# Kernel tuning notes

Measured on AMD Instinct MI355X. Metric: run time of the kernel, lower is better.

The kernel has to match this reference:

```python
import jax, jax.numpy as jnp
import numpy as np

N_AGENTS = 32
UNIT_DIM = 32
STATE_DIM = 1200
N_HEAD = 8
EMBED = 64
KEY_HID = 2 * EMBED
HYPER = 256
V_HID = 4 * EMBED
ATTEND_REG_COEF = 0.001
BS, T = 128, 32


def setup_inputs() -> dict:
    key = jax.random.key(0)
    ks = jax.random.split(key, 12)
    def lin(k, shape, fan_in):
        return jax.random.normal(k, shape, jnp.float32) / np.sqrt(fan_in)
    return dict(
        agent_qs=jax.random.normal(ks[0], (BS, T, N_AGENTS), jnp.float32),
        states=jax.random.normal(ks[1], (BS, T, STATE_DIM), jnp.float32),
        actions=jax.random.randint(ks[2], (BS, T, N_AGENTS), 0, 20),
        sel_W1=lin(ks[3], (N_HEAD, HYPER, STATE_DIM), STATE_DIM),
        sel_b1=jnp.zeros((N_HEAD, HYPER), jnp.float32),
        sel_W2=lin(ks[4], (N_HEAD, EMBED, HYPER), HYPER),
        key_W1=lin(ks[5], (N_HEAD, KEY_HID, UNIT_DIM + 1), UNIT_DIM + 1),
        key_b1=jnp.zeros((N_HEAD, KEY_HID), jnp.float32),
        key_W2=lin(ks[6], (N_HEAD, EMBED, KEY_HID), KEY_HID),
        wh_W1=lin(ks[7], (HYPER, STATE_DIM), STATE_DIM),
        wh_b1=jnp.zeros((HYPER,), jnp.float32),
        wh_W2=lin(ks[8], (N_HEAD, HYPER), HYPER),
        wh_b2=jnp.zeros((N_HEAD,), jnp.float32),
        v_W1=lin(ks[9], (V_HID, STATE_DIM), STATE_DIM),
        v_b1=jnp.zeros((V_HID,), jnp.float32),
        v_W2=lin(ks[10], (1, V_HID), V_HID),
        v_b2=jnp.zeros((1,), jnp.float32),
    )


def reference(agent_qs, states, actions, sel_W1, sel_b1, sel_W2, key_W1, key_b1, key_W2,
              wh_W1, wh_b1, wh_W2, wh_b2, v_W1, v_b1, v_W2, v_b2):
    bs = agent_qs.shape[0]
    s = states.reshape(-1, STATE_DIM)                       # (B, S), B = bs*T
    B = s.shape[0]
    units = s[:, :UNIT_DIM * N_AGENTS].reshape(B, N_AGENTS, UNIT_DIM)  # (B, A, U)
    q = agent_qs.reshape(B, N_AGENTS)                       # (B, A)
    # nonlinear=True: append each agent's q to its unit features
    units = jnp.concatenate([units, q[:, :, None]], axis=2)  # (B, A, U+1)
    a = actions.reshape(B, N_AGENTS)
    # selector hypernets (all heads batched): (B, H, E)
    h1 = jax.nn.relu(jnp.einsum('bs,hes->bhe', s, sel_W1) + sel_b1[None])
    sel = jnp.einsum('bhe,hde->bhd', h1, sel_W2)
    # key hypernets (all heads x all agents batched): (B, H, A, E)
    k1 = jax.nn.relu(jnp.einsum('bau,hku->bhak', units, key_W1) + key_b1[None, :, None, :])
    keys = jnp.einsum('bhak,hdk->bhad', k1, key_W2)
    logits = jnp.einsum('bhd,bhad->bha', sel, keys)          # unscaled, used for regularizer
    scaled = logits / np.sqrt(EMBED)
    scaled = jnp.where(a[:, None, :] == 0, -99999999.0, scaled)  # mask_dead
    w = jax.nn.softmax(scaled, axis=2)                       # (B, H, A)
    head_q = jnp.einsum('ba,bha->bh', q, w)                  # (B, H)
    # weighted_head + state_bias
    wh = jnp.abs(jax.nn.relu(s @ wh_W1.T + wh_b1) @ wh_W2.T + wh_b2)  # (B, H)
    v = (jax.nn.relu(s @ v_W1.T + v_b1) @ v_W2.T + v_b2)[:, 0]        # (B,)
    y = (wh * head_q).sum(axis=1) + v
    q_tot = y.reshape(bs, -1, 1)
    # sum over heads of per-head mean of squared (unscaled) logits
    attend_mag_regs = ATTEND_REG_COEF * (logits ** 2).mean(axis=(0, 2)).sum()
    # per-head entropy: sum over agents, mean over batch
    head_entropies = -(jnp.log(w + 1e-8) * w).sum(axis=2).mean(axis=0)  # (H,)
    return q_tot, attend_mag_regs, head_entropies
```

## Files before the change

### kernel.cpp

```cpp
#include <hip/hip_runtime.h>

#define B_TOT 4096
#define SDIM  1200
#define KPAD  1216
#define NA    32
#define NH    8
#define EMB   64
#define KHID  128
#define HYP   256
#define NSEL  2048
#define NTOT  2560

#define WS_H1BF 0
#define WS_M    (WS_H1BF + (size_t)B_TOT * NTOT / 2)
#define WS_LG   (WS_M    + (size_t)B_TOT * NH * KHID)
#define WS_PART (WS_LG   + (size_t)B_TOT * NH * NA)
#define WS_P2   (WS_PART + (size_t)B_TOT * 16)
#define WS_ABF  (WS_P2   + (size_t)32 * 16)
#define WS_WBF  (WS_ABF  + (size_t)B_TOT * KPAD / 2)
#define WS_KW32 (WS_WBF  + (size_t)NTOT * KPAD / 2)
#define WS_W32F (WS_KW32 + (size_t)1024 * 32 / 2)
#define WS_M2T  (WS_W32F + (size_t)1024)
#define WS_UBF  (WS_M2T  + (size_t)NH * KHID * HYP / 2)

typedef __attribute__((ext_vector_type(8))) short short8v;
typedef __attribute__((ext_vector_type(4))) float floatx4;

#define GLL16(gsrc, ldst) __builtin_amdgcn_global_load_lds( \
    (const __attribute__((address_space(1))) unsigned int*)(gsrc), \
    (__attribute__((address_space(3))) unsigned int*)(ldst), 16, 0, 0)

__device__ __forceinline__ ushort f2bf(float x) {
    unsigned u = __builtin_bit_cast(unsigned, x);
    unsigned r = (u + 0x7FFFu + ((u >> 16) & 1u)) >> 16;
    return (ushort)r;
}
__device__ __forceinline__ float bf2f(ushort u) {
    unsigned x = ((unsigned)u) << 16;
    return __builtin_bit_cast(float, x);
}

__global__ __launch_bounds__(256) void k_cvt_states(
    const float* __restrict__ src, ushort* __restrict__ dst)
{
    const size_t g = (size_t)blockIdx.x * 256 + threadIdx.x;
    if (g >= (size_t)B_TOT * (KPAD / 4)) return;
    const int row = (int)(g / (KPAD / 4));
    const int c4  = (int)(g % (KPAD / 4)) * 4;
    ushort4 o = {0, 0, 0, 0};
    if (c4 < SDIM) {
        float4 v = *(const float4*)(src + (size_t)row * SDIM + c4);
        o.x = f2bf(v.x); o.y = f2bf(v.y); o.z = f2bf(v.z); o.w = f2bf(v.w);
    }
    *(ushort4*)(dst + (size_t)row * KPAD + c4) = o;
}

__global__ __launch_bounds__(256) void k_cvt_w(
    const float* __restrict__ sel_W1, const float* __restrict__ wh_W1,
    const float* __restrict__ v_W1, ushort* __restrict__ dst)
{
    const size_t g = (size_t)blockIdx.x * 256 + threadIdx.x;
    if (g >= (size_t)NTOT * (KPAD / 4)) return;
    const int row = (int)(g / (KPAD / 4));
    const int c4  = (int)(g % (KPAD / 4)) * 4;
    const float* src = (row < NSEL)       ? (sel_W1 + (size_t)row * SDIM)
                     : (row < NSEL + HYP) ? (wh_W1 + (size_t)(row - NSEL) * SDIM)
                                          : (v_W1  + (size_t)(row - NSEL - HYP) * SDIM);
    ushort4 o = {0, 0, 0, 0};
    if (c4 < SDIM) {
        float4 v = *(const float4*)(src + c4);
        o.x = f2bf(v.x); o.y = f2bf(v.y); o.z = f2bf(v.z); o.w = f2bf(v.w);
    }
    *(ushort4*)(dst + (size_t)row * KPAD + c4) = o;
}

__global__ __launch_bounds__(256) void k_cvt_units(
    const float* __restrict__ states, ushort* __restrict__ dst)
{
    const int row = blockIdx.x * 256 + threadIdx.x;
    if (row >= B_TOT * NA) return;
    const int b = row >> 5, a = row & 31;
    const float* s = states + (size_t)b * SDIM + a * 32;
    ushort o[32];
    #pragma unroll
    for (int j = 0; j < 8; ++j) {
        float4 v = *(const float4*)(s + j * 4);
        o[j * 4 + 0] = f2bf(v.x); o[j * 4 + 1] = f2bf(v.y);
        o[j * 4 + 2] = f2bf(v.z); o[j * 4 + 3] = f2bf(v.w);
    }
    const int swz = (row >> 1) & 3;
    #pragma unroll
    for (int c = 0; c < 4; ++c)
        *(short8v*)(dst + (size_t)row * 32 + (c ^ swz) * 8) = *(short8v*)&o[c * 8];
}

__global__ __launch_bounds__(256) void k_cvt_kw2(
    const float* __restrict__ key_W1, ushort* __restrict__ kw32,
    float* __restrict__ w32f)
{
    const int row = blockIdx.x * 256 + threadIdx.x;
    if (row >= 1024) return;
    const float* srcr = key_W1 + (size_t)row * 33;
    ushort o[32];
    #pragma unroll
    for (int u = 0; u < 32; ++u) o[u] = f2bf(srcr[u]);
    const int swz = (row >> 1) & 3;
    #pragma unroll
    for (int c = 0; c < 4; ++c)
        *(short8v*)(kw32 + (size_t)row * 32 + (c ^ swz) * 8) = *(short8v*)&o[c * 8];
    w32f[row] = srcr[32];
}

__global__ __launch_bounds__(256) void k_m2(
    const float* __restrict__ sel_W2, const float* __restrict__ key_W2,
    ushort* __restrict__ M2T)
{
    __shared__ float ssel[EMB * HYP];
    __shared__ float skey[EMB][8];
    const int t  = threadIdx.x;
    const int h  = blockIdx.x;
    const int k0 = blockIdx.y * 8;

    const float4* sw = (const float4*)(sel_W2 + (size_t)h * EMB * HYP);
    #pragma unroll
    for (int j = 0; j < 16; ++j)
        ((float4*)ssel)[j * 256 + t] = sw[j * 256 + t];
    if (t < EMB) {
        #pragma unroll
        for (int kk = 0; kk < 8; ++kk)
            skey[t][kk] = key_W2[((size_t)h * EMB + t) * KHID + k0 + kk];
    }
    __syncthreads();

    const int e = t;
    float acc[8] = {};
    for (int d = 0; d < EMB; ++d) {
        const float sv = ssel[d * HYP + e];
        #pragma unroll
        for (int kk = 0; kk < 8; ++kk)
            acc[kk] = fmaf(sv, skey[d][kk], acc[kk]);
    }
    #pragma unroll
    for (int kk = 0; kk < 8; ++kk)
        M2T[((size_t)h * KHID + k0 + kk) * HYP + e] = f2bf(acc[kk]);
}

#define BK 32
__global__ __launch_bounds__(256) void k_gemm1_mfma(
    const ushort* __restrict__ Abf, const ushort* __restrict__ Wbf,
    const float* __restrict__ sel_b1, const float* __restrict__ wh_b1,
    const float* __restrict__ v_b1, ushort* __restrict__ h1bf)
{
    __shared__ ushort As[128 * BK];
    __shared__ ushort Bs[128 * BK];
    const int tid = threadIdx.x;
    const int l   = tid & 63;
    const int w   = tid >> 6;
    const int wM  = w >> 1, wN = w & 1;
    const int arow0 = blockIdx.y * 128;
    const int nrow0 = blockIdx.x * 128;

    const int srow = tid >> 2;
    const int skof = (tid & 3) * 8;
    const ushort* gA = Abf + (size_t)(arow0 + srow) * KPAD + skof;
    const ushort* gB = Wbf + (size_t)(nrow0 + srow) * KPAD + skof;
    ushort* lA = &As[srow * BK + skof];
    ushort* lB = &Bs[srow * BK + skof];

    floatx4 acc[4][4] = {};

    for (int k0 = 0; k0 < KPAD; k0 += BK) {
        GLL16(gA + k0, lA);
        GLL16(gA + (size_t)64 * KPAD + k0, lA + 64 * BK);
        GLL16(gB + k0, lB);
        GLL16(gB + (size_t)64 * KPAD + k0, lB + 64 * BK);
        __syncthreads();

        const int kch = (l >> 4) * 8;
        short8v av[4], bv[4];
        #pragma unroll
        for (int mi = 0; mi < 4; ++mi)
            av[mi] = *(const short8v*)&As[(wM * 64 + mi * 16 + (l & 15)) * BK + kch];
        #pragma unroll
        for (int ni = 0; ni < 4; ++ni)
            bv[ni] = *(const short8v*)&Bs[(wN * 64 + ni * 16 + (l & 15)) * BK + kch];
        #pragma unroll
        for (int mi = 0; mi < 4; ++mi)
            #pragma unroll
            for (int ni = 0; ni < 4; ++ni)
                acc[mi][ni] = __builtin_amdgcn_mfma_f32_16x16x32_bf16(
                    av[mi], bv[ni], acc[mi][ni], 0, 0, 0);
        __syncthreads();
    }

    float bias_n[4];
    #pragma unroll
    for (int ni = 0; ni < 4; ++ni) {
        const int col = nrow0 + wN * 64 + ni * 16 + (l & 15);
        bias_n[ni] = (col < NSEL)       ? sel_b1[col]
                   : (col < NSEL + HYP) ? wh_b1[col - NSEL]
                                        : v_b1[col - NSEL - HYP];
    }
    #pragma unroll
    for (int mi = 0; mi < 4; ++mi) {
        const int row = arow0 + wM * 64 + mi * 16 + (l >> 4) * 4;
        #pragma unroll
        for (int ni = 0; ni < 4; ++ni) {
            const int col = nrow0 + wN * 64 + ni * 16 + (l & 15);
            #pragma unroll
            for (int r = 0; r < 4; ++r)
                h1bf[(size_t)(row + r) * NTOT + col] =
                    f2bf(fmaxf(acc[mi][ni][r] + bias_n[ni], 0.f));
        }
    }
}

__global__ __launch_bounds__(256) void k_m_mfma(
    const ushort* __restrict__ h1bf, const ushort* __restrict__ M2T,
    float* __restrict__ m_out)
{
    __shared__ ushort As[128 * BK];
    __shared__ ushort Bs[128 * BK];
    const int tid = threadIdx.x;
    const int l   = tid & 63;
    const int w   = tid >> 6;
    const int wM  = w >> 1, wN = w & 1;
    const int h     = blockIdx.x;
    const int brow0 = blockIdx.y * 128;

    const int srow = tid >> 2;
    const int skof = (tid & 3) * 8;
    const ushort* gA = h1bf + (size_t)(brow0 + srow) * NTOT + h * HYP + skof;
    const ushort* gB = M2T + ((size_t)h * KHID + srow) * HYP + skof;
    ushort* lA = &As[srow * BK + skof];
    ushort* lB = &Bs[srow * BK + skof];

    floatx4 acc[4][4] = {};

    for (int k0 = 0; k0 < HYP; k0 += BK) {
        GLL16(gA + k0, lA);
        GLL16(gA + (size_t)64 * NTOT + k0, lA + 64 * BK);
        GLL16(gB + k0, lB);
        GLL16(gB + (size_t)64 * HYP + k0, lB + 64 * BK);
        __syncthreads();

        const int kch = (l >> 4) * 8;
        short8v av[4], bv[4];
        #pragma unroll
        for (int mi = 0; mi < 4; ++mi)
            av[mi] = *(const short8v*)&As[(wM * 64 + mi * 16 + (l & 15)) * BK + kch];
        #pragma unroll
        for (int ni = 0; ni < 4; ++ni)
            bv[ni] = *(const short8v*)&Bs[(wN * 64 + ni * 16 + (l & 15)) * BK + kch];
        #pragma unroll
        for (int mi = 0; mi < 4; ++mi)
            #pragma unroll
            for (int ni = 0; ni < 4; ++ni)
                acc[mi][ni] = __builtin_amdgcn_mfma_f32_16x16x32_bf16(
                    av[mi], bv[ni], acc[mi][ni], 0, 0, 0);
        __syncthreads();
    }

    #pragma unroll
    for (int mi = 0; mi < 4; ++mi) {
        const int row = brow0 + wM * 64 + mi * 16 + (l >> 4) * 4;
        #pragma unroll
        for (int ni = 0; ni < 4; ++ni) {
            const int col = wN * 64 + ni * 16 + (l & 15);
            #pragma unroll
            for (int r = 0; r < 4; ++r)
                m_out[((size_t)(row + r) * NH + h) * KHID + col] = acc[mi][ni][r];
        }
    }
}

__global__ __launch_bounds__(256) void k_logits_mfma(
    const ushort* __restrict__ Ubf, const ushort* __restrict__ KW32,
    const float* __restrict__ W32f, const float* __restrict__ key_b1,
    const float* __restrict__ agent_qs, const float* __restrict__ m_in,
    float* __restrict__ logits)
{
    __shared__ ushort Us[128 * 32];
    __shared__ ushort Wd[2][128 * 32];
    __shared__ float m_lds[4 * NH * KHID];
    __shared__ float b1_lds[1024];
    __shared__ float w32_lds[1024];
    __shared__ float q_lds[128];
    __shared__ float red[128][2];
    const int tid = threadIdx.x;
    const int l = tid & 63;
    const int w = tid >> 6;
    const int wM = w >> 1, wN = w & 1;
    const int r0 = blockIdx.x * 128;
    const int b0 = blockIdx.x * 4;

    #pragma unroll
    for (int c = 0; c < 2; ++c)
        GLL16(Ubf + (size_t)r0 * 32 + c * 2048 + tid * 8, &Us[c * 2048 + tid * 8]);
    #pragma unroll
    for (int c = 0; c < 2; ++c)
        GLL16(KW32 + c * 2048 + tid * 8, &Wd[0][c * 2048 + tid * 8]);
    #pragma unroll
    for (int c = 0; c < 4; ++c)
        GLL16(m_in + (size_t)b0 * NH * KHID + c * 1024 + tid * 4,
              &m_lds[c * 1024 + tid * 4]);
    GLL16(key_b1 + tid * 4, &b1_lds[tid * 4]);
    GLL16(W32f + tid * 4, &w32_lds[tid * 4]);
    if (tid < 128) q_lds[tid] = agent_qs[r0 + tid];
    __syncthreads();

    short8v av[4];
    float4 qv[4];
    #pragma unroll
    for (int mi = 0; mi < 4; ++mi) {
        const int row = wM * 64 + mi * 16 + (l & 15);
        av[mi] = *(const short8v*)&Us[row * 32 + (((l >> 4)) ^ ((row >> 1) & 3)) * 8];
        qv[mi] = *(const float4*)&q_lds[wM * 64 + mi * 16 + (l >> 4) * 4];
    }
    const int bi0 = wM * 2, bi1 = wM * 2 + 1;

    int cur = 0;
    for (int h = 0; h < NH; ++h) {
        if (h < 7) {
            #pragma unroll
            for (int c = 0; c < 2; ++c)
                GLL16(KW32 + (size_t)(h + 1) * 4096 + c * 2048 + tid * 8,
                      &Wd[cur ^ 1][c * 2048 + tid * 8]);
        }
        short8v bv[4];
        float b1r[4], w32r[4], m0r[4], m1r[4];
        #pragma unroll
        for (int ni = 0; ni < 4; ++ni) {
            const int k = wN * 64 + ni * 16 + (l & 15);
            bv[ni] = *(const short8v*)&Wd[cur][k * 32 + (((l >> 4)) ^ ((k >> 1) & 3)) * 8];
            b1r[ni]  = b1_lds[h * 128 + k];
            w32r[ni] = w32_lds[h * 128 + k];
            m0r[ni]  = m_lds[bi0 * 1024 + h * 128 + k];
            m1r[ni]  = m_lds[bi1 * 1024 + h * 128 + k];
        }
        floatx4 acc[4][4] = {};
        #pragma unroll
        for (int mi = 0; mi < 4; ++mi)
            #pragma unroll
            for (int ni = 0; ni < 4; ++ni)
                acc[mi][ni] = __builtin_amdgcn_mfma_f32_16x16x32_bf16(
                    av[mi], bv[ni], acc[mi][ni], 0, 0, 0);

        #pragma unroll
        for (int mi = 0; mi < 4; ++mi) {
            const int rowbase = wM * 64 + mi * 16 + (l >> 4) * 4;
            float s0 = 0.f, s1 = 0.f, s2 = 0.f, s3 = 0.f;
            #pragma unroll
            for (int ni = 0; ni < 4; ++ni) {
                const float mv = (mi < 2) ? m0r[ni] : m1r[ni];
                s0 = fmaf(fmaxf(fmaf(qv[mi].x, w32r[ni], acc[mi][ni][0] + b1r[ni]), 0.f), mv, s0);
                s1 = fmaf(fmaxf(fmaf(qv[mi].y, w32r[ni], acc[mi][ni][1] + b1r[ni]), 0.f), mv, s1);
                s2 = fmaf(fmaxf(fmaf(qv[mi].z, w32r[ni], acc[mi][ni][2] + b1r[ni]), 0.f), mv, s2);
                s3 = fmaf(fmaxf(fmaf(qv[mi].w, w32r[ni], acc[mi][ni][3] + b1r[ni]), 0.f), mv, s3);
            }
            #pragma unroll
            for (int off = 8; off >= 1; off >>= 1) {
                s0 += __shfl_xor(s0, off);
                s1 += __shfl_xor(s1, off);
                s2 += __shfl_xor(s2, off);
                s3 += __shfl_xor(s3, off);
            }
            if ((l & 15) == 0) {
                red[rowbase + 0][wN] = s0;
                red[rowbase + 1][wN] = s1;
                red[rowbase + 2][wN] = s2;
                red[rowbase + 3][wN] = s3;
            }
        }
        __syncthreads();
        if (tid < 128) {
            const float sum = red[tid][0] + red[tid][1];
            logits[((size_t)(b0 + (tid >> 5)) * NH + h) * NA + (tid & 31)] = sum;
        }
        __syncthreads();
        cur ^= 1;
    }
}

__global__ __launch_bounds__(256) void k_softmax(
    const float* __restrict__ logits, const float* __restrict__ agent_qs,
    const int* __restrict__ actions, const ushort* __restrict__ h1bf,
    const float* __restrict__ wh_W2, const float* __restrict__ wh_b2,
    const float* __restrict__ v_W2, const float* __restrict__ v_b2,
    float* __restrict__ out, float* __restrict__ part)
{
    __shared__ float qs[NA];
    __shared__ int   act_s[NA];
    __shared__ float whs[NH];
    __shared__ float hq[NH];
    __shared__ float vred[4];
    const int b = blockIdx.x, t = threadIdx.x;
    if (t < NA) {
        qs[t]    = agent_qs[(size_t)b * NA + t];
        act_s[t] = actions[(size_t)b * NA + t];
    }
    const int h = t >> 5, a = t & 31;
    {
        float acc = 0.f;
        #pragma unroll
        for (int j = 0; j < 8; ++j) {
            const int e = a + 32 * j;
            acc = fmaf(bf2f(h1bf[(size_t)b * NTOT + NSEL + e]),
                       wh_W2[h * HYP + e], acc);
        }
        #pragma unroll
        for (int off = 16; off >= 1; off >>= 1) acc += __shfl_xor(acc, off, 32);
        if (a == 0) whs[h] = fabsf(acc + wh_b2[h]);
    }
    {
        float acc = bf2f(h1bf[(size_t)b * NTOT + NSEL + HYP + t]) * v_W2[t];
        #pragma unroll
        for (int off = 32; off >= 1; off >>= 1) acc += __shfl_xor(acc, off);
        if ((t & 63) == 0) vred[t >> 6] = acc;
    }
    __syncthreads();

    const float lg = logits[((size_t)b * NH + h) * NA + a];
    float sc = (act_s[a] == 0) ? -99999999.0f : lg * 0.125f;

    float mx = sc;
    #pragma unroll
    for (int off = 16; off >= 1; off >>= 1) mx = fmaxf(mx, __shfl_xor(mx, off, 32));
    const float e = expf(sc - mx);
    float sum = e;
    #pragma unroll
    for (int off = 16; off >= 1; off >>= 1) sum += __shfl_xor(sum, off, 32);
    const float wgt = e / sum;

    float r_sq  = lg * lg;
    float r_hq  = qs[a] * wgt;
    float r_ent = -wgt * logf(wgt + 1e-8f);
    #pragma unroll
    for (int off = 16; off >= 1; off >>= 1) {
        r_sq  += __shfl_xor(r_sq,  off, 32);
        r_hq  += __shfl_xor(r_hq,  off, 32);
        r_ent += __shfl_xor(r_ent, off, 32);
    }
    if (a == 0) {
        hq[h] = r_hq;
        part[(size_t)b * 16 + h]     = r_sq;
        part[(size_t)b * 16 + 8 + h] = r_ent;
    }
    __syncthreads();
    if (t == 0) {
        float y = vred[0] + vred[1] + vred[2] + vred[3] + v_b2[0];
        #pragma unroll
        for (int i = 0; i < NH; ++i) y = fmaf(whs[i], hq[i], y);
        out[b] = y;
    }
}

__global__ __launch_bounds__(256) void k_final_s1(
    const float* __restrict__ part, float* __restrict__ part2)
{
    __shared__ float red[16][17];
    const int t = threadIdx.x;
    const int c = t & 15, rl = t >> 4;
    const int rbase = blockIdx.x * 128 + rl;
    float v0 = 0.f, v1 = 0.f, v2 = 0.f, v3 = 0.f;
    #pragma unroll
    for (int j = 0; j < 8; j += 4) {
        v0 += part[(size_t)(rbase + (j + 0) * 16) * 16 + c];
        v1 += part[(size_t)(rbase + (j + 1) * 16) * 16 + c];
        v2 += part[(size_t)(rbase + (j + 2) * 16) * 16 + c];
        v3 += part[(size_t)(rbase + (j + 3) * 16) * 16 + c];
    }
    red[rl][c] = (v0 + v1) + (v2 + v3);
    __syncthreads();
    if (t < 16) {
        float s = 0.f;
        #pragma unroll
        for (int i = 0; i < 16; ++i) s += red[i][t];
        part2[blockIdx.x * 16 + t] = s;
    }
}

__global__ __launch_bounds__(256) void k_final_s2(
    const float* __restrict__ part2, float* __restrict__ out)
{
    __shared__ float red[16][17];
    __shared__ float tot[16];
    const int t = threadIdx.x;
    {
        const int g = t >> 4, c = t & 15;
        red[g][c] = part2[t] + part2[t + 256];
    }
    __syncthreads();
    if (t < 16) {
        float s = 0.f;
        #pragma unroll
        for (int i = 0; i < 16; ++i) s += red[i][t];
        tot[t] = s;
    }
    __syncthreads();
    if (t == 0) {
        float s = 0.f;
        #pragma unroll
        for (int i = 0; i < 8; ++i) s += tot[i];
        out[B_TOT] = 0.001f * (s / (float)((size_t)B_TOT * NA));
    }
    if (t >= 8 && t < 16)
        out[B_TOT + 1 + (t - 8)] = tot[t] / (float)B_TOT;
}

extern "C" void kernel_launch(void* const* d_in, const int* in_sizes, int n_in,
                              void* d_out, int out_size, void* d_ws, size_t ws_size,
                              hipStream_t stream) {
    (void)in_sizes; (void)n_in; (void)out_size; (void)ws_size;
    const float* agent_qs = (const float*)d_in[0];
    const float* states   = (const float*)d_in[1];
    const int*   actions  = (const int*)d_in[2];
    const float* sel_W1   = (const float*)d_in[3];
    const float* sel_b1   = (const float*)d_in[4];
    const float* sel_W2   = (const float*)d_in[5];
    const float* key_W1   = (const float*)d_in[6];
    const float* key_b1   = (const float*)d_in[7];
    const float* key_W2   = (const float*)d_in[8];
    const float* wh_W1    = (const float*)d_in[9];
    const float* wh_b1    = (const float*)d_in[10];
    const float* wh_W2    = (const float*)d_in[11];
    const float* wh_b2    = (const float*)d_in[12];
    const float* v_W1     = (const float*)d_in[13];
    const float* v_b1     = (const float*)d_in[14];
    const float* v_W2     = (const float*)d_in[15];
    const float* v_b2     = (const float*)d_in[16];

    float* out = (float*)d_out;
    float* ws  = (float*)d_ws;
    ushort* h1bf  = (ushort*)(ws + WS_H1BF);
    float* m_buf  = ws + WS_M;
    float* lg_buf = ws + WS_LG;
    float* part   = ws + WS_PART;
    float* part2  = ws + WS_P2;
    ushort* Abf   = (ushort*)(ws + WS_ABF);
    ushort* Wbf   = (ushort*)(ws + WS_WBF);
    ushort* KW32  = (ushort*)(ws + WS_KW32);
    float*  W32f  = ws + WS_W32F;
    ushort* M2T   = (ushort*)(ws + WS_M2T);
    ushort* Ubf   = (ushort*)(ws + WS_UBF);

    {
        const int groups_a = B_TOT * (KPAD / 4);
        const int groups_w = NTOT * (KPAD / 4);
        k_cvt_states<<<(groups_a + 255) / 256, 256, 0, stream>>>(states, Abf);
        k_cvt_w<<<(groups_w + 255) / 256, 256, 0, stream>>>(sel_W1, wh_W1, v_W1, Wbf);
        k_cvt_kw2<<<4, 256, 0, stream>>>(key_W1, KW32, W32f);
        k_cvt_units<<<(B_TOT * NA + 255) / 256, 256, 0, stream>>>(states, Ubf);
        k_m2<<<dim3(NH, KHID / 8), 256, 0, stream>>>(sel_W2, key_W2, M2T);
    }
    k_gemm1_mfma<<<dim3(NTOT / 128, B_TOT / 128), 256, 0, stream>>>(
        Abf, Wbf, sel_b1, wh_b1, v_b1, h1bf);
    k_m_mfma<<<dim3(NH, B_TOT / 128), 256, 0, stream>>>(h1bf, M2T, m_buf);
    k_logits_mfma<<<dim3((B_TOT * NA) / 128), 256, 0, stream>>>(
        Ubf, KW32, W32f, key_b1, agent_qs, m_buf, lg_buf);
    k_softmax<<<dim3(B_TOT), 256, 0, stream>>>(
        lg_buf, agent_qs, actions, h1bf, wh_W2, wh_b2, v_W2, v_b2, out, part);
    k_final_s1<<<32, 256, 0, stream>>>(part, part2);
    k_final_s2<<<1, 256, 0, stream>>>(part2, out);
}
```

Baseline: 130.6 us.

## Remove LDS staging and barriers from logits kernel, one wave per batch row

```diff
diff --git a/kernel.cpp b/kernel.cpp
--- a/kernel.cpp
+++ b/kernel.cpp
@@ -88,10 +88,9 @@
         o[j * 4 + 0] = f2bf(v.x); o[j * 4 + 1] = f2bf(v.y);
         o[j * 4 + 2] = f2bf(v.z); o[j * 4 + 3] = f2bf(v.w);
     }
-    const int swz = (row >> 1) & 3;
     #pragma unroll
     for (int c = 0; c < 4; ++c)
-        *(short8v*)(dst + (size_t)row * 32 + (c ^ swz) * 8) = *(short8v*)&o[c * 8];
+        *(short8v*)(dst + (size_t)row * 32 + c * 8) = *(short8v*)&o[c * 8];
 }
 
 __global__ __launch_bounds__(256) void k_cvt_kw2(
@@ -104,10 +103,9 @@
     ushort o[32];
     #pragma unroll
     for (int u = 0; u < 32; ++u) o[u] = f2bf(srcr[u]);
-    const int swz = (row >> 1) & 3;
     #pragma unroll
     for (int c = 0; c < 4; ++c)
-        *(short8v*)(kw32 + (size_t)row * 32 + (c ^ swz) * 8) = *(short8v*)&o[c * 8];
+        *(short8v*)(kw32 + (size_t)row * 32 + c * 8) = *(short8v*)&o[c * 8];
     w32f[row] = srcr[32];
 }
 
@@ -280,83 +278,52 @@
     const float* __restrict__ agent_qs, const float* __restrict__ m_in,
     float* __restrict__ logits)
 {
-    __shared__ ushort Us[128 * 32];
-    __shared__ ushort Wd[2][128 * 32];
-    __shared__ float m_lds[4 * NH * KHID];
-    __shared__ float b1_lds[1024];
-    __shared__ float w32_lds[1024];
-    __shared__ float q_lds[128];
-    __shared__ float red[128][2];
     const int tid = threadIdx.x;
-    const int l = tid & 63;
-    const int w = tid >> 6;
-    const int wM = w >> 1, wN = w & 1;
-    const int r0 = blockIdx.x * 128;
-    const int b0 = blockIdx.x * 4;
-
-    #pragma unroll
-    for (int c = 0; c < 2; ++c)
-        GLL16(Ubf + (size_t)r0 * 32 + c * 2048 + tid * 8, &Us[c * 2048 + tid * 8]);
-    #pragma unroll
-    for (int c = 0; c < 2; ++c)
-        GLL16(KW32 + c * 2048 + tid * 8, &Wd[0][c * 2048 + tid * 8]);
-    #pragma unroll
-    for (int c = 0; c < 4; ++c)
-        GLL16(m_in + (size_t)b0 * NH * KHID + c * 1024 + tid * 4,
-              &m_lds[c * 1024 + tid * 4]);
-    GLL16(key_b1 + tid * 4, &b1_lds[tid * 4]);
-    GLL16(W32f + tid * 4, &w32_lds[tid * 4]);
-    if (tid < 128) q_lds[tid] = agent_qs[r0 + tid];
-    __syncthreads();
-
-    short8v av[4];
-    float4 qv[4];
-    #pragma unroll
-    for (int mi = 0; mi < 4; ++mi) {
-        const int row = wM * 64 + mi * 16 + (l & 15);
-        av[mi] = *(const short8v*)&Us[row * 32 + (((l >> 4)) ^ ((row >> 1) & 3)) * 8];
-        qv[mi] = *(const float4*)&q_lds[wM * 64 + mi * 16 + (l >> 4) * 4];
-    }
-    const int bi0 = wM * 2, bi1 = wM * 2 + 1;
-
-    int cur = 0;
+    const int l   = tid & 63;
+    const int w   = tid >> 6;
+    const int b   = blockIdx.x * 4 + w;
+    const int urow0 = b * NA;
+
+    short8v av[2];
+    float4 qv[2];
+    #pragma unroll
+    for (int mi = 0; mi < 2; ++mi) {
+        av[mi] = *(const short8v*)(
+            Ubf + (size_t)(urow0 + mi * 16 + (l & 15)) * 32 + (l >> 4) * 8);
+        qv[mi] = *(const float4*)(
+            agent_qs + (size_t)b * NA + mi * 16 + (l >> 4) * 4);
+    }
+
     for (int h = 0; h < NH; ++h) {
-        if (h < 7) {
-            #pragma unroll
-            for (int c = 0; c < 2; ++c)
-                GLL16(KW32 + (size_t)(h + 1) * 4096 + c * 2048 + tid * 8,
-                      &Wd[cur ^ 1][c * 2048 + tid * 8]);
+        short8v bv[8];
+        float b1r[8], w32r[8], mr[8];
+        #pragma unroll
+        for (int ni = 0; ni < 8; ++ni) {
+            const int k = ni * 16 + (l & 15);
+            bv[ni]   = *(const short8v*)(
+                KW32 + ((size_t)h * KHID + k) * 32 + (l >> 4) * 8);
+            b1r[ni]  = key_b1[h * KHID + k];
+            w32r[ni] = W32f[h * KHID + k];
+            mr[ni]   = m_in[((size_t)b * NH + h) * KHID + k];
         }
-        short8v bv[4];
-        float b1r[4], w32r[4], m0r[4], m1r[4];
-        #pragma unroll
-        for (int ni = 0; ni < 4; ++ni) {
-            const int k = wN * 64 + ni * 16 + (l & 15);
-            bv[ni] = *(const short8v*)&Wd[cur][k * 32 + (((l >> 4)) ^ ((k >> 1) & 3)) * 8];
-            b1r[ni]  = b1_lds[h * 128 + k];
-            w32r[ni] = w32_lds[h * 128 + k];
-            m0r[ni]  = m_lds[bi0 * 1024 + h * 128 + k];
-            m1r[ni]  = m_lds[bi1 * 1024 + h * 128 + k];
-        }
-        floatx4 acc[4][4] = {};
-        #pragma unroll
-        for (int mi = 0; mi < 4; ++mi)
-            #pragma unroll
-            for (int ni = 0; ni < 4; ++ni)
+        floatx4 acc[2][8] = {};
+        #pragma unroll
+        for (int mi = 0; mi < 2; ++mi)
+            #pragma unroll
+            for (int ni = 0; ni < 8; ++ni)
                 acc[mi][ni] = __builtin_amdgcn_mfma_f32_16x16x32_bf16(
                     av[mi], bv[ni], acc[mi][ni], 0, 0, 0);
 
         #pragma unroll
-        for (int mi = 0; mi < 4; ++mi) {
-            const int rowbase = wM * 64 + mi * 16 + (l >> 4) * 4;
+        for (int mi = 0; mi < 2; ++mi) {
             float s0 = 0.f, s1 = 0.f, s2 = 0.f, s3 = 0.f;
             #pragma unroll
-            for (int ni = 0; ni < 4; ++ni) {
-                const float mv = (mi < 2) ? m0r[ni] : m1r[ni];
-                s0 = fmaf(fmaxf(fmaf(qv[mi].x, w32r[ni], acc[mi][ni][0] + b1r[ni]), 0.f), mv, s0);
-                s1 = fmaf(fmaxf(fmaf(qv[mi].y, w32r[ni], acc[mi][ni][1] + b1r[ni]), 0.f), mv, s1);
-                s2 = fmaf(fmaxf(fmaf(qv[mi].z, w32r[ni], acc[mi][ni][2] + b1r[ni]), 0.f), mv, s2);
-                s3 = fmaf(fmaxf(fmaf(qv[mi].w, w32r[ni], acc[mi][ni][3] + b1r[ni]), 0.f), mv, s3);
+            for (int ni = 0; ni < 8; ++ni) {
+                const float b1v = b1r[ni], wv = w32r[ni], mv = mr[ni];
+                s0 = fmaf(fmaxf(fmaf(qv[mi].x, wv, acc[mi][ni][0] + b1v), 0.f), mv, s0);
+                s1 = fmaf(fmaxf(fmaf(qv[mi].y, wv, acc[mi][ni][1] + b1v), 0.f), mv, s1);
+                s2 = fmaf(fmaxf(fmaf(qv[mi].z, wv, acc[mi][ni][2] + b1v), 0.f), mv, s2);
+                s3 = fmaf(fmaxf(fmaf(qv[mi].w, wv, acc[mi][ni][3] + b1v), 0.f), mv, s3);
             }
             #pragma unroll
             for (int off = 8; off >= 1; off >>= 1) {
@@ -366,19 +333,11 @@
                 s3 += __shfl_xor(s3, off);
             }
             if ((l & 15) == 0) {
-                red[rowbase + 0][wN] = s0;
-                red[rowbase + 1][wN] = s1;
-                red[rowbase + 2][wN] = s2;
-                red[rowbase + 3][wN] = s3;
+                float4 o = {s0, s1, s2, s3};
+                *(float4*)(logits + ((size_t)b * NH + h) * NA
+                           + mi * 16 + (l >> 4) * 4) = o;
             }
         }
-        __syncthreads();
-        if (tid < 128) {
-            const float sum = red[tid][0] + red[tid][1];
-            logits[((size_t)(b0 + (tid >> 5)) * NH + h) * NA + (tid & 31)] = sum;
-        }
-        __syncthreads();
-        cur ^= 1;
     }
 }
 
@@ -556,7 +515,7 @@
     k_gemm1_mfma<<<dim3(NTOT / 128, B_TOT / 128), 256, 0, stream>>>(
         Abf, Wbf, sel_b1, wh_b1, v_b1, h1bf);
     k_m_mfma<<<dim3(NH, B_TOT / 128), 256, 0, stream>>>(h1bf, M2T, m_buf);
-    k_logits_mfma<<<dim3((B_TOT * NA) / 128), 256, 0, stream>>>(
+    k_logits_mfma<<<dim3(B_TOT / 4), 256, 0, stream>>>(
         Ubf, KW32, W32f, key_b1, agent_qs, m_buf, lg_buf);
     k_softmax<<<dim3(B_TOT), 256, 0, stream>>>(
         lg_buf, agent_qs, actions, h1bf, wh_W2, wh_b2, v_W2, v_b2, out, part);
```

New measurement: 123.1 us. 5.7% less time.
